# Kernel optimization log

Hardware: AMD Instinct MI355X
Metric: run time of the kernel (lower is better)

## Reference

```python
import jax, jax.numpy as jnp
import numpy as np

B, T, C = 16, 1024, 768
H = 12
D = C // H  # 64 head dim


def setup_inputs() -> dict:
    key = jax.random.key(0)
    k1, k2, k3, k4, k5 = jax.random.split(key, 5)
    s = 0.02
    return {
        "x": jax.random.normal(k1, (B, T, C), dtype=jnp.float32),
        "w_attn": jax.random.normal(k2, (C, 3 * C), dtype=jnp.float32) * s,
        "b_attn": jax.random.normal(k3, (3 * C,), dtype=jnp.float32) * s,
        "w_proj": jax.random.normal(k4, (C, C), dtype=jnp.float32) * s,
        "b_proj": jax.random.normal(k5, (C,), dtype=jnp.float32) * s,
    }


def reference(x, w_attn, b_attn, w_proj, b_proj):
    Bc, Tc, Cc = x.shape
    qkv = x @ w_attn + b_attn  # [B,T,3C]
    q, k, v = jnp.split(qkv, 3, axis=-1)
    # [B,T,C] -> [B,H,T,D]
    q = q.reshape(Bc, Tc, H, D).transpose(0, 2, 1, 3)
    k = k.reshape(Bc, Tc, H, D).transpose(0, 2, 1, 3)
    v = v.reshape(Bc, Tc, H, D).transpose(0, 2, 1, 3)
    scale = 1.0 / np.sqrt(D).astype(np.float32)
    atn = jnp.einsum("bhqd,bhkd->bhqk", q, k) * scale
    causal = jnp.tril(jnp.ones((Tc, Tc), dtype=bool))
    atn = jnp.where(causal[None, None], atn, -jnp.inf)
    atn = jax.nn.softmax(atn, axis=-1)
    y = jnp.einsum("bhqk,bhkd->bhqd", atn, v)
    y = y.transpose(0, 2, 1, 3).reshape(Bc, Tc, Cc)
    return y @ w_proj + b_proj
```

## Files before the change

### kernel.cpp

```cpp
#include <hip/hip_runtime.h>
#include <hip/hip_bf16.h>

typedef __attribute__((ext_vector_type(4))) float f32x4;
typedef __attribute__((ext_vector_type(8))) short s16x8;
typedef __attribute__((ext_vector_type(4))) short s16x4;

#define AS1 __attribute__((address_space(1)))
#define AS3 __attribute__((address_space(3)))

__device__ __forceinline__ short f2bf(float f) {
    union { float f; unsigned u; } a; a.f = f;
    unsigned r = a.u + 0x7fff + ((a.u >> 16) & 1);
    return (short)(r >> 16);
}

__device__ __forceinline__ unsigned pk_bf16(float a, float b) {
    unsigned r;
    asm("v_cvt_pk_bf16_f32 %0, %1, %2" : "=v"(r) : "v"(a), "v"(b));
    return r;
}


__global__ __launch_bounds__(256) void convert_f32_bf16(const float* __restrict__ in,
                                                        short* __restrict__ out, int n4) {
    int i = blockIdx.x * 256 + threadIdx.x;
    if (i < n4) {
        f32x4 v = *(const f32x4*)(in + (long)i * 4);
        s16x4 o;
        o.x = f2bf(v.x); o.y = f2bf(v.y); o.z = f2bf(v.z); o.w = f2bf(v.w);
        *(s16x4*)(out + (long)i * 4) = o;
    }
}

__global__ __launch_bounds__(256) void transpose_w(const float* __restrict__ src,
                                                   short* __restrict__ dst, int K, int N) {
    __shared__ short t[64][65];
    int k0 = blockIdx.x * 64, n0 = blockIdx.y * 64;
    int tid = threadIdx.x;
    for (int i = tid; i < 64 * 64; i += 256) {
        int r = i >> 6, c = i & 63;
        t[r][c] = f2bf(src[(long)(k0 + r) * N + n0 + c]);
    }
    __syncthreads();
    for (int i = tid; i < 64 * 64; i += 256) {
        int r = i >> 6, c = i & 63;
        dst[(long)(n0 + r) * K + k0 + c] = t[c][r];
    }
}

__global__ __launch_bounds__(256) void transpose_vp(const short* __restrict__ vp,
                                                    short* __restrict__ vt) {
    __shared__ short t[64][72];
    int t0 = blockIdx.x * 64;
    int g = blockIdx.y;
    int tid = threadIdx.x;
#pragma unroll
    for (int i = 0; i < 2; ++i) {
        int j = tid + i * 256;
        int r = j >> 3, c = j & 7;
        s16x8 v = *(const s16x8*)(vp + ((long)g * 1024 + t0 + r) * 64 + c * 8);
#pragma unroll
        for (int e = 0; e < 8; ++e) t[c * 8 + e][r] = v[e];
    }
    __syncthreads();
#pragma unroll
    for (int i = 0; i < 2; ++i) {
        int j = tid + i * 256;
        int r = j >> 3, c = j & 7;
        *(s16x8*)(vt + ((long)g * 64 + r) * 1024 + t0 + c * 8) = *(const s16x8*)&t[r][c * 8];
    }
}


template <int MODE>
__global__ __launch_bounds__(256) void gemm_bt(const short* __restrict__ A,
                                               const short* __restrict__ BT,
                                               const float* __restrict__ bias,
                                               float* __restrict__ outF,
                                               short* __restrict__ q_,
                                               short* __restrict__ k_,
                                               short* __restrict__ v_,
                                               int M, int N, int K) {
    __shared__ short lA[2 * 64 * 64];
    __shared__ short lB[2 * 64 * 64];
    int tid = threadIdx.x;
    int lane = tid & 63, w = tid >> 6;
    int wr = w >> 1, wc = w & 1;
    int lo = lane & 15, hi = lane >> 4;

    int bid = blockIdx.x;
    int swz = (bid & 7) * ((int)gridDim.x >> 3) + (bid >> 3);
    int NX = N >> 7;
    int bx = swz % NX, by = swz / NX;
    int m0 = by * 128, n0 = bx * 128;

    f32x4 acc[4][4];
#pragma unroll
    for (int i = 0; i < 4; ++i)
#pragma unroll
        for (int j = 0; j < 4; ++j) acc[i][j] = (f32x4){0.f, 0.f, 0.f, 0.f};

    const short* Abase = A + (long)m0 * K;
    const short* Bbase = BT + (long)n0 * K;

    int lr = lane >> 3;
    int cc = (lane & 7) ^ lr;
    int growoff = cc >> 2;
    int gcol = (cc & 3) * 8;

    int srlo = lo >> 1;
    int rpar = (lo & 1) << 2;

    for (int k0 = 0; k0 < K; k0 += 64) {
        __syncthreads();
#pragma unroll
        for (int kk = 0; kk < 2; ++kk)
#pragma unroll
            for (int j = 0; j < 2; ++j) {
                int sr = w * 16 + j * 8 + lr;
                long grow = (long)(sr * 2 + growoff);
                const short* ga = Abase + grow * K + k0 + kk * 32 + gcol;
                const short* gb = Bbase + grow * K + k0 + kk * 32 + gcol;
                short* da = lA + kk * 4096 + (w * 16 + j * 8) * 64;
                short* db = lB + kk * 4096 + (w * 16 + j * 8) * 64;
                __builtin_amdgcn_global_load_lds((const AS1 void*)ga, (AS3 void*)da, 16, 0, 0);
                __builtin_amdgcn_global_load_lds((const AS1 void*)gb, (AS3 void*)db, 16, 0, 0);
            }
        __syncthreads();

#pragma unroll
        for (int kk = 0; kk < 2; ++kk) {
            s16x8 a[4], b[4];
#pragma unroll
            for (int mi = 0; mi < 4; ++mi)
                a[mi] = *(const s16x8*)(lA + kk * 4096 + (wr * 32 + mi * 8 + srlo) * 64 +
                                        ((rpar + hi) ^ srlo) * 8);
#pragma unroll
            for (int ni = 0; ni < 4; ++ni)
                b[ni] = *(const s16x8*)(lB + kk * 4096 + (wc * 32 + ni * 8 + srlo) * 64 +
                                        ((rpar + hi) ^ srlo) * 8);
#pragma unroll
            for (int mi = 0; mi < 4; ++mi)
#pragma unroll
                for (int ni = 0; ni < 4; ++ni)
                    acc[mi][ni] = __builtin_amdgcn_mfma_f32_16x16x32_bf16(a[mi], b[ni], acc[mi][ni], 0, 0, 0);
        }
    }

    float bs[4];
#pragma unroll
    for (int ni = 0; ni < 4; ++ni) bs[ni] = bias[n0 + wc * 64 + ni * 16 + lo];

    if (MODE == 1) {
        int blk = (n0 + wc * 64) >> 6;
        int part = (blk >= 24) ? 2 : (blk >= 12 ? 1 : 0);
        int hh = blk - part * 12;
        short* dst = (part == 0) ? q_ : (part == 1) ? k_ : v_;
        float scl = (part == 0) ? 0.180336880f : 1.0f;
        int bidx = m0 >> 10;
        int trow0 = (m0 & 1023) + wr * 64;
        long gb_ = ((long)(bidx * 12 + hh)) << 16;
#pragma unroll
        for (int mi = 0; mi < 4; ++mi)
#pragma unroll
            for (int ni = 0; ni < 4; ++ni)
#pragma unroll
                for (int r = 0; r < 4; ++r) {
                    int trow = trow0 + mi * 16 + hi * 4 + r;
                    float v = (acc[mi][ni][r] + bs[ni]) * scl;
                    dst[gb_ + (long)trow * 64 + ni * 16 + lo] = f2bf(v);
                }
    } else {
#pragma unroll
        for (int mi = 0; mi < 4; ++mi)
#pragma unroll
            for (int ni = 0; ni < 4; ++ni)
#pragma unroll
                for (int r = 0; r < 4; ++r) {
                    int gm = m0 + wr * 64 + mi * 16 + hi * 4 + r;
                    int gn = n0 + wc * 64 + ni * 16 + lo;
                    outF[(long)gm * N + gn] = acc[mi][ni][r] + bs[ni];
                }
    }
}


__device__ __forceinline__ void qk_softmax(const short* __restrict__ Kb_,
                                           int kv0, int qb0, bool diag,
                                           s16x8 bq0, s16x8 bq1,
                                           f32x4 (&ov)[4], float& mrun, float& lrun,
                                           s16x8 (&ap)[2],
                                           int lo, int hi, int hi2, int sA, int sB,
                                           int sl0, int sl1) {
    f32x4 s[4];
    __builtin_amdgcn_s_setprio(1);
#pragma unroll
    for (int n = 0; n < 4; ++n) {
        const short* kr = Kb_ + (n * 16 + lo) * 64;
        s16x8 kf0 = *(const s16x8*)(kr + sl0);
        s16x8 kf1 = *(const s16x8*)(kr + sl1);
        f32x4 t = (f32x4){0.f, 0.f, 0.f, 0.f};
        t = __builtin_amdgcn_mfma_f32_16x16x32_bf16(kf0, bq0, t, 0, 0, 0);
        t = __builtin_amdgcn_mfma_f32_16x16x32_bf16(kf1, bq1, t, 0, 0, 0);
        s[n] = t;
    }
    __builtin_amdgcn_s_setprio(0);

    int qglob = qb0 + lo;
    if (diag) {
#pragma unroll
        for (int n = 0; n < 4; ++n)
#pragma unroll
            for (int r = 0; r < 4; ++r)
                if (kv0 + n * 16 + hi * 4 + r > qglob) s[n][r] = -3.0e38f;
    }
    float mx = s[0][0];
#pragma unroll
    for (int n = 0; n < 4; ++n)
#pragma unroll
        for (int r = 0; r < 4; ++r) mx = fmaxf(mx, s[n][r]);
    mx = fmaxf(mx, __shfl_xor(mx, 16));
    mx = fmaxf(mx, __shfl_xor(mx, 32));
    float mn = fmaxf(mrun, mx);
    float alpha = exp2f(mrun - mn);
    mrun = mn;
    float rs = 0.f;
#pragma unroll
    for (int n = 0; n < 4; ++n)
#pragma unroll
        for (int r = 0; r < 4; ++r) {
            float p = exp2f(s[n][r] - mn);
            s[n][r] = p;
            rs += p;
        }
    rs += __shfl_xor(rs, 16);
    rs += __shfl_xor(rs, 32);
    lrun = lrun * alpha + rs;
#pragma unroll
    for (int nd = 0; nd < 4; ++nd)
#pragma unroll
        for (int r = 0; r < 4; ++r) ov[nd][r] *= alpha;

    unsigned W[4][2];
#pragma unroll
    for (int n = 0; n < 4; ++n) {
        W[n][0] = pk_bf16(s[n][0], s[n][1]);
        W[n][1] = pk_bf16(s[n][2], s[n][3]);
    }
#pragma unroll
    for (int kc = 0; kc < 2; ++kc) {
        unsigned a0 = __shfl(W[kc * 2][0], sA), b0 = __shfl(W[kc * 2 + 1][0], sA);
        unsigned a1 = __shfl(W[kc * 2][1], sA), b1 = __shfl(W[kc * 2 + 1][1], sA);
        unsigned a2 = __shfl(W[kc * 2][0], sB), b2 = __shfl(W[kc * 2 + 1][0], sB);
        unsigned a3 = __shfl(W[kc * 2][1], sB), b3 = __shfl(W[kc * 2 + 1][1], sB);
        union { unsigned u[4]; s16x8 v; } cv;
        cv.u[0] = hi2 ? b0 : a0;
        cv.u[1] = hi2 ? b1 : a1;
        cv.u[2] = hi2 ? b2 : a2;
        cv.u[3] = hi2 ? b3 : a3;
        ap[kc] = cv.v;
    }
}

__device__ __forceinline__ void pv_accum(const short* __restrict__ Vb_,
                                         const s16x8 (&ap)[2], f32x4 (&ov)[4],
                                         int lo, int sl0, int sl1) {
    __builtin_amdgcn_s_setprio(1);
#pragma unroll
    for (int nd = 0; nd < 4; ++nd) {
        const short* vr = Vb_ + (nd * 16 + lo) * 64;
        s16x8 av0 = *(const s16x8*)(vr + sl0);
        s16x8 av1 = *(const s16x8*)(vr + sl1);
        ov[nd] = __builtin_amdgcn_mfma_f32_16x16x32_bf16(av0, ap[0], ov[nd], 0, 0, 0);
        ov[nd] = __builtin_amdgcn_mfma_f32_16x16x32_bf16(av1, ap[1], ov[nd], 0, 0, 0);
    }
    __builtin_amdgcn_s_setprio(0);
}

__device__ __forceinline__ void store_out(const f32x4 (&ov)[4], float lrun,
                                          long rowbase, int qb0, int h,
                                          int lo, int hi, short* __restrict__ y) {
    float inv = 1.0f / lrun;
    long row = (rowbase + qb0 + lo) * 768 + h * 64;
#pragma unroll
    for (int nd = 0; nd < 4; ++nd)
#pragma unroll
        for (int j2 = 0; j2 < 2; ++j2) {
            unsigned pv = pk_bf16(ov[nd][2 * j2] * inv, ov[nd][2 * j2 + 1] * inv);
            *(unsigned*)(y + row + nd * 16 + hi * 4 + 2 * j2) = pv;
        }
}

__global__ __launch_bounds__(256) void flash_attn8(const short* __restrict__ qpk,
                                                   const short* __restrict__ kpk,
                                                   const short* __restrict__ vtg,
                                                   short* __restrict__ y) {
    __shared__ short Kb[2][4096];
    __shared__ short Vb[4096];

    int d = blockIdx.x;
    int qp = d / 192, g = d % 192;
    int h = g % 12, b = g / 12;
    int tid = threadIdx.x, lane = tid & 63, w = tid >> 6;
    int lo = lane & 15, hi = lane >> 4, hi2 = hi >> 1;
    long rowbase = (long)b * 1024;
    const short* kb_g = kpk + (long)g * 65536;
    const short* vt_g = vtg + (long)g * 65536;
    int sA = ((hi & 1) * 2) * 16 + lo, sB = sA + 16;

    int rl = lane >> 3;
    int cs8 = (((lane & 7) ^ rl)) * 8;
    int r0 = w * 8 + rl;
    int sl0 = (hi ^ (lo & 7)) * 8;
    int sl1 = ((hi + 4) ^ (lo & 7)) * 8;

    int qbA = qp * 64 + w * 16;
    int qbB = (15 - qp) * 64 + w * 16;

    f32x4 ov[4];
    float mrun = -3.0e38f, lrun = 0.f;
#pragma unroll
    for (int nd = 0; nd < 4; ++nd) ov[nd] = (f32x4){0.f, 0.f, 0.f, 0.f};
    s16x8 bq0, bq1;
    {
        const short* qrow = qpk + ((long)g * 1024 + qbA + lo) * 64;
        bq0 = *(const s16x8*)(qrow + hi * 8);
        bq1 = *(const s16x8*)(qrow + 32 + hi * 8);
    }

#define STAGE_K(kv0_, buf_)                                                                  \
    do {                                                                                     \
        _Pragma("unroll")                                                                    \
        for (int i_ = 0; i_ < 2; ++i_) {                                                     \
            int r_ = i_ * 32 + r0;                                                           \
            __builtin_amdgcn_global_load_lds(                                                \
                (const AS1 void*)(kb_g + (long)((kv0_) + r_) * 64 + cs8),                    \
                (AS3 void*)(Kb[buf_] + (i_ * 32 + w * 8) * 64), 16, 0, 0);                   \
        }                                                                                    \
    } while (0)

#define STAGE_V(kv0_)                                                                        \
    do {                                                                                     \
        _Pragma("unroll")                                                                    \
        for (int i_ = 0; i_ < 2; ++i_) {                                                     \
            int r_ = i_ * 32 + r0;                                                           \
            __builtin_amdgcn_global_load_lds(                                                \
                (const AS1 void*)(vt_g + (long)r_ * 1024 + (kv0_) + cs8),                    \
                (AS3 void*)(Vb + (i_ * 32 + w * 8) * 64), 16, 0, 0);                         \
        }                                                                                    \
    } while (0)

    STAGE_K(0, 0);
    STAGE_V(0);
    __syncthreads();

    int cur = 0;
    for (int u = 0; u < 17; ++u) {
        int nu = u + 1;
        int nkv0 = (nu <= qp) ? nu * 64 : (nu - qp - 1) * 64;
        if (nu < 17) STAGE_K(nkv0, cur ^ 1);

        bool phaseA = (u <= qp);
        int kv0 = phaseA ? u * 64 : (u - qp - 1) * 64;
        int qb0 = phaseA ? qbA : qbB;
        bool diag = phaseA ? (u == qp) : (u == 16);

        s16x8 ap[2];
        qk_softmax(Kb[cur], kv0, qb0, diag, bq0, bq1, ov, mrun, lrun, ap,
                   lo, hi, hi2, sA, sB, sl0, sl1);

        __syncthreads();
        __builtin_amdgcn_sched_barrier(0);

        pv_accum(Vb, ap, ov, lo, sl0, sl1);

        if (phaseA && u == qp) {
            store_out(ov, lrun, rowbase, qbA, h, lo, hi, y);
            const short* qrow = qpk + ((long)g * 1024 + qbB + lo) * 64;
            bq0 = *(const s16x8*)(qrow + hi * 8);
            bq1 = *(const s16x8*)(qrow + 32 + hi * 8);
#pragma unroll
            for (int nd = 0; nd < 4; ++nd) ov[nd] = (f32x4){0.f, 0.f, 0.f, 0.f};
            mrun = -3.0e38f; lrun = 0.f;
        }

        __builtin_amdgcn_s_barrier();
        __builtin_amdgcn_sched_barrier(0);
        if (nu < 17) STAGE_V(nkv0);
        cur ^= 1;
    }
    store_out(ov, lrun, rowbase, qbB, h, lo, hi, y);
#undef STAGE_K
#undef STAGE_V
}


extern "C" void kernel_launch(void* const* d_in, const int* in_sizes, int n_in,
                              void* d_out, int out_size, void* d_ws, size_t ws_size,
                              hipStream_t stream) {
    const float* x      = (const float*)d_in[0];
    const float* w_attn = (const float*)d_in[1];
    const float* b_attn = (const float*)d_in[2];
    const float* w_proj = (const float*)d_in[3];
    const float* b_proj = (const float*)d_in[4];

    char* ws = (char*)d_ws;
    short* x_bf = (short*)ws;
    short* qpk  = (short*)(ws + 25165824);
    short* kpk  = (short*)(ws + 50331648);
    short* vpk  = (short*)(ws + 75497472);
    short* yb   = (short*)(ws + 100663296);
    short* waT  = (short*)(ws + 125829120);
    short* wpT  = (short*)(ws + 129368064);
    short* vt   = x_bf;

    convert_f32_bf16<<<dim3(12288), dim3(256), 0, stream>>>(x, x_bf, 3145728);
    transpose_w<<<dim3(12, 36), dim3(256), 0, stream>>>(w_attn, waT, 768, 2304);
    transpose_w<<<dim3(12, 12), dim3(256), 0, stream>>>(w_proj, wpT, 768, 768);
    gemm_bt<1><<<dim3(2304), dim3(256), 0, stream>>>(x_bf, waT, b_attn,
                                                     (float*)nullptr, qpk, kpk, vpk,
                                                     16384, 2304, 768);
    transpose_vp<<<dim3(16, 192), dim3(256), 0, stream>>>(vpk, vt);
    flash_attn8<<<dim3(1536), dim3(256), 0, stream>>>(qpk, kpk, vt, yb);
    gemm_bt<0><<<dim3(768), dim3(256), 0, stream>>>(yb, wpT, b_proj,
                                                    (float*)d_out, (short*)nullptr,
                                                    (short*)nullptr, (short*)nullptr,
                                                    16384, 768, 768);
}
```

Measured before the change: 211.0 us.

## Fuse V transpose into QKV GEMM epilogue and add lazy softmax rescaling

The QKV GEMM epilogue now writes V directly in transposed [head, d, t] layout with 4-wide vector stores, so the separate transpose_vp kernel and its extra global round trip are removed. In the attention softmax, the running max is only updated (and O/l rescaled) when some lane's new max exceeds the old by more than 8 in log2 units, skipping most rescale multiplies. The max reduction is also rewritten as a balanced tree for shorter dependency chains. Lazy rescaling lets exp2 arguments reach up to 2^8, which bounds growth but slightly changes numerics.

```diff
diff --git a/kernel.cpp b/kernel.cpp
--- a/kernel.cpp
+++ b/kernel.cpp
@@ -45,29 +45,6 @@
     for (int i = tid; i < 64 * 64; i += 256) {
         int r = i >> 6, c = i & 63;
         dst[(long)(n0 + r) * K + k0 + c] = t[c][r];
-    }
-}
-
-__global__ __launch_bounds__(256) void transpose_vp(const short* __restrict__ vp,
-                                                    short* __restrict__ vt) {
-    __shared__ short t[64][72];
-    int t0 = blockIdx.x * 64;
-    int g = blockIdx.y;
-    int tid = threadIdx.x;
-#pragma unroll
-    for (int i = 0; i < 2; ++i) {
-        int j = tid + i * 256;
-        int r = j >> 3, c = j & 7;
-        s16x8 v = *(const s16x8*)(vp + ((long)g * 1024 + t0 + r) * 64 + c * 8);
-#pragma unroll
-        for (int e = 0; e < 8; ++e) t[c * 8 + e][r] = v[e];
-    }
-    __syncthreads();
-#pragma unroll
-    for (int i = 0; i < 2; ++i) {
-        int j = tid + i * 256;
-        int r = j >> 3, c = j & 7;
-        *(s16x8*)(vt + ((long)g * 64 + r) * 1024 + t0 + c * 8) = *(const s16x8*)&t[r][c * 8];
     }
 }
 
@@ -155,21 +132,36 @@
         int blk = (n0 + wc * 64) >> 6;
         int part = (blk >= 24) ? 2 : (blk >= 12 ? 1 : 0);
         int hh = blk - part * 12;
-        short* dst = (part == 0) ? q_ : (part == 1) ? k_ : v_;
-        float scl = (part == 0) ? 0.180336880f : 1.0f;
         int bidx = m0 >> 10;
         int trow0 = (m0 & 1023) + wr * 64;
         long gb_ = ((long)(bidx * 12 + hh)) << 16;
-#pragma unroll
-        for (int mi = 0; mi < 4; ++mi)
-#pragma unroll
-            for (int ni = 0; ni < 4; ++ni)
-#pragma unroll
-                for (int r = 0; r < 4; ++r) {
-                    int trow = trow0 + mi * 16 + hi * 4 + r;
-                    float v = (acc[mi][ni][r] + bs[ni]) * scl;
-                    dst[gb_ + (long)trow * 64 + ni * 16 + lo] = f2bf(v);
+        if (part == 2) {
+#pragma unroll
+            for (int mi = 0; mi < 4; ++mi)
+#pragma unroll
+                for (int ni = 0; ni < 4; ++ni) {
+                    s16x4 o;
+                    o.x = f2bf(acc[mi][ni][0] + bs[ni]);
+                    o.y = f2bf(acc[mi][ni][1] + bs[ni]);
+                    o.z = f2bf(acc[mi][ni][2] + bs[ni]);
+                    o.w = f2bf(acc[mi][ni][3] + bs[ni]);
+                    int tq = trow0 + mi * 16 + hi * 4;
+                    *(s16x4*)(v_ + gb_ + (long)(ni * 16 + lo) * 1024 + tq) = o;
                 }
+        } else {
+            short* dst = (part == 0) ? q_ : k_;
+            float scl = (part == 0) ? 0.180336880f : 1.0f;
+#pragma unroll
+            for (int mi = 0; mi < 4; ++mi)
+#pragma unroll
+                for (int ni = 0; ni < 4; ++ni)
+#pragma unroll
+                    for (int r = 0; r < 4; ++r) {
+                        int trow = trow0 + mi * 16 + hi * 4 + r;
+                        float v = (acc[mi][ni][r] + bs[ni]) * scl;
+                        dst[gb_ + (long)trow * 64 + ni * 16 + lo] = f2bf(v);
+                    }
+        }
     } else {
 #pragma unroll
         for (int mi = 0; mi < 4; ++mi)
@@ -214,32 +206,35 @@
             for (int r = 0; r < 4; ++r)
                 if (kv0 + n * 16 + hi * 4 + r > qglob) s[n][r] = -3.0e38f;
     }
-    float mx = s[0][0];
-#pragma unroll
-    for (int n = 0; n < 4; ++n)
-#pragma unroll
-        for (int r = 0; r < 4; ++r) mx = fmaxf(mx, s[n][r]);
+    float mx = fmaxf(fmaxf(fmaxf(s[0][0], s[0][1]), fmaxf(s[0][2], s[0][3])),
+                     fmaxf(fmaxf(s[1][0], s[1][1]), fmaxf(s[1][2], s[1][3])));
+    mx = fmaxf(mx, fmaxf(fmaxf(fmaxf(s[2][0], s[2][1]), fmaxf(s[2][2], s[2][3])),
+                         fmaxf(fmaxf(s[3][0], s[3][1]), fmaxf(s[3][2], s[3][3]))));
     mx = fmaxf(mx, __shfl_xor(mx, 16));
     mx = fmaxf(mx, __shfl_xor(mx, 32));
-    float mn = fmaxf(mrun, mx);
-    float alpha = exp2f(mrun - mn);
-    mrun = mn;
+    if (!__all(mx - mrun <= 8.0f)) {
+        float mn = fmaxf(mrun, mx);
+        float alpha = exp2f(mrun - mn);
+        mrun = mn;
+        lrun *= alpha;
+#pragma unroll
+        for (int nd = 0; nd < 4; ++nd)
+#pragma unroll
+            for (int r = 0; r < 4; ++r) ov[nd][r] *= alpha;
+    }
+    float m = mrun;
     float rs = 0.f;
 #pragma unroll
     for (int n = 0; n < 4; ++n)
 #pragma unroll
         for (int r = 0; r < 4; ++r) {
-            float p = exp2f(s[n][r] - mn);
+            float p = exp2f(s[n][r] - m);
             s[n][r] = p;
             rs += p;
         }
     rs += __shfl_xor(rs, 16);
     rs += __shfl_xor(rs, 32);
-    lrun = lrun * alpha + rs;
-#pragma unroll
-    for (int nd = 0; nd < 4; ++nd)
-#pragma unroll
-        for (int r = 0; r < 4; ++r) ov[nd][r] *= alpha;
+    lrun += rs;
 
     unsigned W[4][2];
 #pragma unroll
@@ -291,7 +286,7 @@
         }
 }
 
-__global__ __launch_bounds__(256) void flash_attn8(const short* __restrict__ qpk,
+__global__ __launch_bounds__(256) void flash_attn9(const short* __restrict__ qpk,
                                                    const short* __restrict__ kpk,
                                                    const short* __restrict__ vtg,
                                                    short* __restrict__ y) {
@@ -408,20 +403,18 @@
     short* x_bf = (short*)ws;
     short* qpk  = (short*)(ws + 25165824);
     short* kpk  = (short*)(ws + 50331648);
-    short* vpk  = (short*)(ws + 75497472);
+    short* vt   = (short*)(ws + 75497472);
     short* yb   = (short*)(ws + 100663296);
     short* waT  = (short*)(ws + 125829120);
     short* wpT  = (short*)(ws + 129368064);
-    short* vt   = x_bf;
 
     convert_f32_bf16<<<dim3(12288), dim3(256), 0, stream>>>(x, x_bf, 3145728);
     transpose_w<<<dim3(12, 36), dim3(256), 0, stream>>>(w_attn, waT, 768, 2304);
     transpose_w<<<dim3(12, 12), dim3(256), 0, stream>>>(w_proj, wpT, 768, 768);
     gemm_bt<1><<<dim3(2304), dim3(256), 0, stream>>>(x_bf, waT, b_attn,
-                                                     (float*)nullptr, qpk, kpk, vpk,
+                                                     (float*)nullptr, qpk, kpk, vt,
                                                      16384, 2304, 768);
-    transpose_vp<<<dim3(16, 192), dim3(256), 0, stream>>>(vpk, vt);
-    flash_attn8<<<dim3(1536), dim3(256), 0, stream>>>(qpk, kpk, vt, yb);
+    flash_attn9<<<dim3(1536), dim3(256), 0, stream>>>(qpk, kpk, vt, yb);
     gemm_bt<0><<<dim3(768), dim3(256), 0, stream>>>(yb, wpT, b_proj,
                                                     (float*)d_out, (short*)nullptr,
                                                     (short*)nullptr, (short*)nullptr,
```

New measurement: 201.3 us (median of 2 runs). 4.6% less time.
